# Performance work log

Hardware: AMD Instinct MI355X
Metric: run time of the kernel (lower is better)

Reference implementation:

```python
import jax, jax.numpy as jnp
import numpy as np

B, N, D = 8, 2048, 8        # batch, nodes, input_dim == hidden_dim
E, DEC = 8, 128             # embedding_dim, decoder_dim


def _leaky(x, slope):
    return jnp.where(x >= 0, x, slope * x)


def _sage(x, attn, inv_deg, w, b):
    # adj transposed on dims (1,2) then left-matmul: new[b,i,d] = sum_j attn[b,j,i] x[b,j,d]
    new_x = jnp.einsum('bji,bjd->bid', attn, x)
    new_x = jnp.matmul(inv_deg, new_x)
    new_x = jnp.matmul(new_x, w)
    self_x = jnp.matmul(x, b)
    c = jnp.concatenate([new_x, self_x], axis=2)
    norm = jnp.sqrt(jnp.sum(c * c, axis=2, keepdims=True))
    return c / jnp.maximum(norm, 1e-12)  # F.normalize(p=2, dim=2)


def setup_inputs():
    key = jax.random.key(0)
    ks = jax.random.split(key, 12)
    x = jax.random.normal(ks[0], (B, N, D), jnp.float32)
    adj = jax.random.randint(ks[1], (B, N, N), 0, 2).astype(jnp.int32)
    deg = jnp.sum(adj.astype(jnp.float32), axis=2)
    inv_deg = jax.vmap(jnp.diag)(1.0 / (deg + 1.0))  # [B,N,N] diagonal
    g = np.sqrt(2.0)  # xavier-style scale stand-in
    W = jax.random.normal(ks[2], (D, D), jnp.float32) * (g / np.sqrt(2 * D))
    a = jax.random.normal(ks[3], (2 * D, 1), jnp.float32) * (g / np.sqrt(2 * D + 1))
    w1 = jax.random.normal(ks[4], (D, D), jnp.float32) * 0.3
    b1 = jax.random.normal(ks[5], (D, D), jnp.float32) * 0.3
    w2 = jax.random.normal(ks[6], (2 * D, D), jnp.float32) * 0.3
    b2 = jax.random.normal(ks[7], (2 * D, D), jnp.float32) * 0.3
    w3 = jax.random.normal(ks[8], (2 * D, E), jnp.float32) * 0.3
    b3 = jax.random.normal(ks[9], (2 * D, E), jnp.float32) * 0.3
    P1 = jax.random.normal(ks[10], (2 * E, DEC), jnp.float32) * 0.1
    P2 = jax.random.normal(ks[11], (DEC, DEC), jnp.float32) * 0.1
    return {"x": x, "adj": adj, "inv_deg": inv_deg, "W": W, "a": a,
            "w1": w1, "b1": b1, "w2": w2, "b2": b2, "w3": w3, "b3": b3,
            "P1": P1, "P2": P2}


def reference(x, adj, inv_deg, W, a, w1, b1, w2, b2, w3, b3, P1, P2):
    h = jnp.matmul(x, W)                          # [B,N,D]
    # e[b,i,j] = leaky(h[b,i].a1 + h[b,j].a2), equivalent to cat+matmul without O(N^2*2D) tensor
    f1 = jnp.matmul(h, a[:D, 0])                  # [B,N]
    f2 = jnp.matmul(h, a[D:, 0])                  # [B,N]
    e = _leaky(f1[:, :, None] + f2[:, None, :], 0.2)
    e = jnp.where(adj > 0, e, jnp.float32(-9e15))
    attn = jax.nn.softmax(e, axis=2)              # [B,N,N]
    out = _leaky(_sage(x, attn, inv_deg, w1, b1), 0.1)
    out = _leaky(_sage(out, attn, inv_deg, w2, b2), 0.1)
    out = _leaky(_sage(out, attn, inv_deg, w3, b3), 0.1)
    da = out[:, N - 2]                            # [B,2E]
    db = out[:, N - 1]
    ypred = jnp.einsum('bi,id,de,je,bj->b', da, P1, P2, P1, db)
    return ypred[:, None]
```

## Files before the change

### kernel.cpp

```cpp
#include <hip/hip_runtime.h>
#include <math.h>

constexpr int CB   = 8;
constexpr int CN   = 2048;
constexpr int CD   = 8;
constexpr int CDEC = 128;
constexpr int CBN  = CB * CN;
constexpr int NWRD = CN / 64;
constexpr int JSP  = 32;
constexpr int JLEN = CN / JSP;

__device__ __forceinline__ float msel_s(unsigned long long m, float p) {
  float r;
  asm("v_cndmask_b32 %0, 0, %1, %2" : "=v"(r) : "v"(p), "s"(m));
  return r;
}
__device__ __forceinline__ float msel(unsigned long long m, int lane, float p) {
  return ((m >> lane) & 1ull) ? p : 0.f;
}

__global__ void prep_k(const float* __restrict__ x,
                       const float* __restrict__ W, const float* __restrict__ a,
                       const float* __restrict__ w1, const float* __restrict__ b1,
                       float4* __restrict__ pk, float4* __restrict__ qk,
                       float* __restrict__ feat1w, float* __restrict__ selfb1) {
  int t = blockIdx.x * blockDim.x + threadIdx.x;
  if (t >= CBN) return;
  const float* xr = x + (size_t)t * CD;
  float h[CD];
#pragma unroll
  for (int d = 0; d < CD; ++d) {
    float s = 0.f;
#pragma unroll
    for (int k = 0; k < CD; ++k) s = fmaf(xr[k], W[k * CD + d], s);
    h[d] = s;
  }
  float s1 = 0.f, s2 = 0.f;
#pragma unroll
  for (int d = 0; d < CD; ++d) { s1 = fmaf(h[d], a[d], s1); s2 = fmaf(h[d], a[CD + d], s2); }
  pk[t] = make_float4(s1, expf(s1), expf(0.2f * s1), 0.f);
  qk[t] = make_float4(s2, expf(s2), expf(0.2f * s2), 0.f);
  float fw[8], fb[8];
#pragma unroll
  for (int o = 0; o < 8; ++o) {
    float sw = 0.f, sb = 0.f;
#pragma unroll
    for (int d = 0; d < CD; ++d) {
      sw = fmaf(xr[d], w1[d * 8 + o], sw);
      sb = fmaf(xr[d], b1[d * 8 + o], sb);
    }
    fw[o] = sw; fb[o] = sb;
  }
  float4* f4 = (float4*)(feat1w + (size_t)t * 8);
  f4[0] = make_float4(fw[0], fw[1], fw[2], fw[3]);
  f4[1] = make_float4(fw[4], fw[5], fw[6], fw[7]);
  float4* s4 = (float4*)(selfb1 + (size_t)t * 8);
  s4[0] = make_float4(fb[0], fb[1], fb[2], fb[3]);
  s4[1] = make_float4(fb[4], fb[5], fb[6], fb[7]);
}

__global__ __launch_bounds__(256) void mask_k(const int* __restrict__ adj,
    float4* __restrict__ pk, const float4* __restrict__ qk,
    unsigned long long* __restrict__ maskT) {
  const int lane = threadIdx.x & 63;
  const int gw2 = blockIdx.x * 4 + (threadIdx.x >> 6);
  const int b = gw2 >> 9;
  const int jw = gw2 & 511;
  const int* ab = adj + (size_t)b * CN * CN;
  const float4* qb = qk + (size_t)b * CN;
  float f1[4];
#pragma unroll
  for (int r = 0; r < 4; ++r) f1[r] = pk[b * CN + jw + 512 * r].x;
  float A[4] = {0.f, 0.f, 0.f, 0.f}, C[4] = {0.f, 0.f, 0.f, 0.f};
  int deg[4] = {0, 0, 0, 0};
  for (int k = 0; k < NWRD; ++k) {
    int i = k * 64 + lane;
    float4 q = qb[i];
    unsigned long long m[4];
#pragma unroll
    for (int r = 0; r < 4; ++r) {
      bool bit = ab[(size_t)(jw + 512 * r) * CN + i] > 0;
      m[r] = __ballot(bit);
      bool cond = (f1[r] + q.x) >= 0.f;
      A[r] += (bit && cond) ? q.y : 0.f;
      C[r] += (bit && !cond) ? q.z : 0.f;
    }
    if (lane == 0) {
#pragma unroll
      for (int r = 0; r < 4; ++r) {
        maskT[((size_t)(b * NWRD + k)) * CN + jw + 512 * r] = m[r];
        deg[r] += __popcll(m[r]);
      }
    }
  }
#pragma unroll
  for (int r = 0; r < 4; ++r) {
#pragma unroll
    for (int off = 32; off; off >>= 1) {
      A[r] += __shfl_down(A[r], off);
      C[r] += __shfl_down(C[r], off);
    }
  }
  if (lane == 0) {
#pragma unroll
    for (int r = 0; r < 4; ++r) {
      int gr = b * CN + jw + 512 * r;
      float4 pj = pk[gr];
      float s = pj.y * A[r] + pj.z * C[r];
      float ga = (s > 0.f) ? pj.y / s : 0.f;
      float gb = (s > 0.f) ? pj.z / s : 0.f;
      float dv = 1.f / (float)(deg[r] + 1);
      pk[gr] = make_float4(pj.x, ga, gb, dv);
    }
  }
}

__global__ __launch_bounds__(256) void aggf_k(const float* __restrict__ feat,
                      const unsigned long long* __restrict__ maskT,
                      const float4* __restrict__ pk, const float4* __restrict__ qk,
                      float* __restrict__ part) {
  const int js = blockIdx.x, ic = blockIdx.y, b = blockIdx.z;
  const int t = threadIdx.x;
  const int w = __builtin_amdgcn_readfirstlane(t >> 6);
  const int i1 = ic * 512 + t, i2 = i1 + 256;
  const int gi1 = b * CN + i1, gi2 = b * CN + i2;
  float4 q1 = qk[gi1], q2 = qk[gi2];
  const unsigned long long* mc1 = maskT + ((size_t)(b * NWRD + ic * 8 + w)) * CN + js * JLEN;
  const unsigned long long* mc2 = maskT + ((size_t)(b * NWRD + ic * 8 + 4 + w)) * CN + js * JLEN;
  const float4* pb = pk + (size_t)b * CN + js * JLEN;
  const float* fb  = feat + ((size_t)b * CN + js * JLEN) * 8;
  float acc1[8], acc2[8];
#pragma unroll
  for (int d = 0; d < 8; ++d) { acc1[d] = 0.f; acc2[d] = 0.f; }
#pragma unroll 4
  for (int jj = 0; jj < JLEN; ++jj) {
    unsigned long long m1 = mc1[jj];
    unsigned long long m2 = mc2[jj];
    float4 pj = pb[jj];
    const float* fr = fb + jj * 8;
    float wA = msel_s(m1, fmaxf(pj.y * q1.y, pj.z * q1.z));
    float wB = msel_s(m2, fmaxf(pj.y * q2.y, pj.z * q2.z));
#pragma unroll
    for (int d = 0; d < 8; ++d) {
      acc1[d] = fmaf(wA, fr[d], acc1[d]);
      acc2[d] = fmaf(wB, fr[d], acc2[d]);
    }
  }
  float4* p1 = (float4*)(part + ((size_t)js * CBN + gi1) * 8);
  float4* p2 = (float4*)(part + ((size_t)js * CBN + gi2) * 8);
  p1[0] = make_float4(acc1[0], acc1[1], acc1[2], acc1[3]);
  p1[1] = make_float4(acc1[4], acc1[5], acc1[6], acc1[7]);
  p2[0] = make_float4(acc2[0], acc2[1], acc2[2], acc2[3]);
  p2[1] = make_float4(acc2[4], acc2[5], acc2[6], acc2[7]);
}

__global__ void epi8_k(const float* __restrict__ part, const float* __restrict__ selfb1,
                       const float4* __restrict__ pk,
                       const float* __restrict__ w2, const float* __restrict__ b2,
                       float* __restrict__ feat2w, float* __restrict__ selfb2) {
  int t = blockIdx.x * blockDim.x + threadIdx.x;
  if (t >= CBN) return;
  float4 a0 = make_float4(0.f, 0.f, 0.f, 0.f), a1 = a0;
  for (int p_ = 0; p_ < JSP; ++p_) {
    const float4* pr = (const float4*)(part + ((size_t)p_ * CBN + t) * 8);
    float4 r0 = pr[0], r1 = pr[1];
    a0.x += r0.x; a0.y += r0.y; a0.z += r0.z; a0.w += r0.w;
    a1.x += r1.x; a1.y += r1.y; a1.z += r1.z; a1.w += r1.w;
  }
  float di = pk[t].w;
  const float4* sb = (const float4*)(selfb1 + (size_t)t * 8);
  float4 s0 = sb[0], s1 = sb[1];
  float c[16] = {a0.x * di, a0.y * di, a0.z * di, a0.w * di,
                 a1.x * di, a1.y * di, a1.z * di, a1.w * di,
                 s0.x, s0.y, s0.z, s0.w, s1.x, s1.y, s1.z, s1.w};
  float nn = 0.f;
#pragma unroll
  for (int k = 0; k < 16; ++k) nn += c[k] * c[k];
  float inv = 1.f / fmaxf(sqrtf(nn), 1e-12f);
  float ff[16];
#pragma unroll
  for (int k = 0; k < 16; ++k) {
    float v = c[k] * inv;
    ff[k] = (v >= 0.f) ? v : 0.1f * v;
  }
  float fw[8], fb[8];
#pragma unroll
  for (int o = 0; o < 8; ++o) {
    float sw = 0.f, sb2_ = 0.f;
#pragma unroll
    for (int d = 0; d < 16; ++d) {
      sw = fmaf(ff[d], w2[d * 8 + o], sw);
      sb2_ = fmaf(ff[d], b2[d * 8 + o], sb2_);
    }
    fw[o] = sw; fb[o] = sb2_;
  }
  float4* f4 = (float4*)(feat2w + (size_t)t * 8);
  f4[0] = make_float4(fw[0], fw[1], fw[2], fw[3]);
  f4[1] = make_float4(fw[4], fw[5], fw[6], fw[7]);
  float4* s4 = (float4*)(selfb2 + (size_t)t * 8);
  s4[0] = make_float4(fb[0], fb[1], fb[2], fb[3]);
  s4[1] = make_float4(fb[4], fb[5], fb[6], fb[7]);
}

__global__ __launch_bounds__(256) void epi16f_k(
    const float* __restrict__ part2, const float* __restrict__ selfb2,
    const unsigned long long* __restrict__ maskT,
    const float4* __restrict__ pk, const float4* __restrict__ qk,
    float* __restrict__ gpart, float* __restrict__ self2) {
  __shared__ float redA[4][16], redB[4][16];
  const int t = threadIdx.x;
  const int lane = t & 63, wv = t >> 6;
  const int gr = blockIdx.x * 256 + t;
  const int b = blockIdx.x >> 3, blk8 = blockIdx.x & 7;
  const int j = gr - b * CN;
  const int ia = CN - 2, ib = CN - 1;
  float4 a0 = make_float4(0.f, 0.f, 0.f, 0.f), a1 = a0;
  for (int p = 0; p < JSP; ++p) {
    const float4* pr = (const float4*)(part2 + ((size_t)p * CBN + gr) * 8);
    float4 r0 = pr[0], r1 = pr[1];
    a0.x += r0.x; a0.y += r0.y; a0.z += r0.z; a0.w += r0.w;
    a1.x += r1.x; a1.y += r1.y; a1.z += r1.z; a1.w += r1.w;
  }
  float4 pj = pk[gr];
  const float4* sb = (const float4*)(selfb2 + (size_t)gr * 8);
  float4 s0 = sb[0], s1 = sb[1];
  float c[16] = {a0.x * pj.w, a0.y * pj.w, a0.z * pj.w, a0.w * pj.w,
                 a1.x * pj.w, a1.y * pj.w, a1.z * pj.w, a1.w * pj.w,
                 s0.x, s0.y, s0.z, s0.w, s1.x, s1.y, s1.z, s1.w};
  float nn = 0.f;
#pragma unroll
  for (int k = 0; k < 16; ++k) nn += c[k] * c[k];
  float inv = 1.f / fmaxf(sqrtf(nn), 1e-12f);
  float ff[16];
#pragma unroll
  for (int k = 0; k < 16; ++k) {
    float v = c[k] * inv;
    ff[k] = (v >= 0.f) ? v : 0.1f * v;
  }
  if (j == ia || j == ib) {
    float* s = self2 + ((size_t)b * 2 + (j == ib ? 1 : 0)) * 16;
#pragma unroll
    for (int d = 0; d < 16; ++d) s[d] = ff[d];
  }
  unsigned long long m = maskT[((size_t)(b * NWRD + (NWRD - 1))) * CN + j];
  float4 qa = qk[b * CN + ia], qb = qk[b * CN + ib];
  float wA = ((m >> 62) & 1ull) ? fmaxf(pj.y * qa.y, pj.z * qa.z) : 0.f;
  float wB = (m >> 63) ? fmaxf(pj.y * qb.y, pj.z * qb.z) : 0.f;
  float accA[16], accB[16];
#pragma unroll
  for (int d = 0; d < 16; ++d) { accA[d] = wA * ff[d]; accB[d] = wB * ff[d]; }
#pragma unroll
  for (int d = 0; d < 16; ++d) {
#pragma unroll
    for (int off = 32; off; off >>= 1) {
      accA[d] += __shfl_down(accA[d], off);
      accB[d] += __shfl_down(accB[d], off);
    }
  }
  if (lane == 0) {
#pragma unroll
    for (int d = 0; d < 16; ++d) { redA[wv][d] = accA[d]; redB[wv][d] = accB[d]; }
  }
  __syncthreads();
  if (t < 32) {
    int row = t >> 4, k = t & 15;
    float s = row ? (redB[0][k] + redB[1][k] + redB[2][k] + redB[3][k])
                  : (redA[0][k] + redA[1][k] + redA[2][k] + redA[3][k]);
    gpart[(((size_t)b * 8 + blk8) * 2 + row) * 16 + k] = s;
  }
}

__global__ __launch_bounds__(CDEC) void dec_k(
    const float* __restrict__ gpart, const float* __restrict__ self2,
    const float4* __restrict__ pk,
    const float* __restrict__ w3, const float* __restrict__ b3,
    const float* __restrict__ P1, const float* __restrict__ P2,
    float* __restrict__ y) {
  __shared__ float agA[16], agB[16], cA[16], cB[16], daF[16], dbF[16];
  __shared__ float vsh[CDEC], red[CDEC];
  const int b = blockIdx.x;
  const int t = threadIdx.x;
  const int ia = CN - 2, ib = CN - 1;
  if (t < 32) {
    int row = t >> 4, k = t & 15;
    float s = 0.f;
#pragma unroll
    for (int blk = 0; blk < 8; ++blk)
      s += gpart[(((size_t)b * 8 + blk) * 2 + row) * 16 + k];
    float dv = pk[b * CN + (row ? ib : ia)].w;
    (row ? agB : agA)[k] = s * dv;
  }
  __syncthreads();
  if (t < 32) {
    int row = t >> 4, k = t & 15;
    const float* ag = row ? agB : agA;
    const float* self = self2 + ((size_t)b * 2 + row) * 16;
    float s = 0.f;
    if (k < 8) {
#pragma unroll
      for (int d = 0; d < 16; ++d) s = fmaf(ag[d], w3[d * 8 + k], s);
    } else {
#pragma unroll
      for (int d = 0; d < 16; ++d) s = fmaf(self[d], b3[d * 8 + (k - 8)], s);
    }
    (row ? cB : cA)[k] = s;
  }
  __syncthreads();
  if (t < 32) {
    int row = t >> 4, k = t & 15;
    const float* c = row ? cB : cA;
    float nn = 0.f;
#pragma unroll
    for (int q = 0; q < 16; ++q) nn += c[q] * c[q];
    float inv = 1.f / fmaxf(sqrtf(nn), 1e-12f);
    float v = c[k] * inv;
    (row ? dbF : daF)[k] = (v >= 0.f) ? v : 0.1f * v;
  }
  __syncthreads();
  float ue = 0.f, ve = 0.f;
#pragma unroll
  for (int i = 0; i < 16; ++i) {
    ue = fmaf(daF[i], P1[i * CDEC + t], ue);
    ve = fmaf(dbF[i], P1[i * CDEC + t], ve);
  }
  vsh[t] = ve;
  __syncthreads();
  float s = 0.f;
  for (int e2 = 0; e2 < CDEC; ++e2) s = fmaf(P2[t * CDEC + e2], vsh[e2], s);
  red[t] = s * ue;
  __syncthreads();
  for (int off = 64; off; off >>= 1) {
    if (t < off) red[t] += red[t + off];
    __syncthreads();
  }
  if (t == 0) y[b] = red[0];
}

extern "C" void kernel_launch(void* const* d_in, const int* in_sizes, int n_in,
                              void* d_out, int out_size, void* d_ws, size_t ws_size,
                              hipStream_t stream) {
  const float* x  = (const float*)d_in[0];
  const int*   adj = (const int*)d_in[1];
  const float* W  = (const float*)d_in[3];
  const float* a  = (const float*)d_in[4];
  const float* w1 = (const float*)d_in[5];
  const float* b1 = (const float*)d_in[6];
  const float* w2 = (const float*)d_in[7];
  const float* b2 = (const float*)d_in[8];
  const float* w3 = (const float*)d_in[9];
  const float* b3 = (const float*)d_in[10];
  const float* P1 = (const float*)d_in[11];
  const float* P2 = (const float*)d_in[12];
  float* y = (float*)d_out;

  char* base = (char*)d_ws;
  size_t off = 0;
  auto alloc = [&](size_t bytes) -> void* {
    void* r = base + off;
    off += (bytes + 255) & ~(size_t)255;
    return r;
  };
  float4* pk = (float4*)alloc(sizeof(float4) * CBN);
  float4* qk = (float4*)alloc(sizeof(float4) * CBN);
  unsigned long long* maskT =
      (unsigned long long*)alloc(sizeof(unsigned long long) * (size_t)CBN * NWRD);
  float* feat1w = (float*)alloc(sizeof(float) * (size_t)CBN * 8);
  float* selfb1 = (float*)alloc(sizeof(float) * (size_t)CBN * 8);
  float* feat2w = (float*)alloc(sizeof(float) * (size_t)CBN * 8);
  float* selfb2 = (float*)alloc(sizeof(float) * (size_t)CBN * 8);
  float* part   = (float*)alloc(sizeof(float) * (size_t)JSP * CBN * 8);
  float* gpart  = (float*)alloc(sizeof(float) * CB * 8 * 2 * 16);
  float* self2  = (float*)alloc(sizeof(float) * CB * 2 * 16);

  hipLaunchKernelGGL(prep_k, dim3(CBN / 256), dim3(256), 0, stream,
                     x, W, a, w1, b1, pk, qk, feat1w, selfb1);
  hipLaunchKernelGGL(mask_k, dim3(1024), dim3(256), 0, stream, adj, pk, qk, maskT);
  hipLaunchKernelGGL(aggf_k, dim3(JSP, 4, CB), dim3(256), 0, stream, feat1w, maskT, pk, qk, part);
  hipLaunchKernelGGL(epi8_k, dim3(CBN / 256), dim3(256), 0, stream,
                     part, selfb1, pk, w2, b2, feat2w, selfb2);
  hipLaunchKernelGGL(aggf_k, dim3(JSP, 4, CB), dim3(256), 0, stream, feat2w, maskT, pk, qk, part);
  hipLaunchKernelGGL(epi16f_k, dim3(CBN / 256), dim3(256), 0, stream,
                     part, selfb2, maskT, pk, qk, gpart, self2);
  hipLaunchKernelGGL(dec_k, dim3(CB), dim3(CDEC), 0, stream,
                     gpart, self2, pk, w3, b3, P1, P2, y);
}
```

Baseline: 96.82 us.

## Fuse prep into mask kernel and decoder into last epilogue via counter

Merges the per-node projection kernel into the mask/softmax-stat kernel. Each block recomputes the q-side logits for the whole batch into shared memory instead of reading them from global memory. Also folds the decoder into the final epilogue: the last block per batch, found with an atomic counter and thread fences, runs the decoder. This removes two launches and the global round trip for q, at the cost of redundant per-block recomputation of 2048 node projections and a counter reset at the start of each run.

Result: slower. 111.2 us (+14.8%).

```diff
diff --git a/kernel.cpp b/kernel.cpp
--- a/kernel.cpp
+++ b/kernel.cpp
@@ -15,75 +15,91 @@
   asm("v_cndmask_b32 %0, 0, %1, %2" : "=v"(r) : "v"(p), "s"(m));
   return r;
 }
-__device__ __forceinline__ float msel(unsigned long long m, int lane, float p) {
-  return ((m >> lane) & 1ull) ? p : 0.f;
-}
-
-__global__ void prep_k(const float* __restrict__ x,
-                       const float* __restrict__ W, const float* __restrict__ a,
-                       const float* __restrict__ w1, const float* __restrict__ b1,
-                       float4* __restrict__ pk, float4* __restrict__ qk,
-                       float* __restrict__ feat1w, float* __restrict__ selfb1) {
-  int t = blockIdx.x * blockDim.x + threadIdx.x;
-  if (t >= CBN) return;
-  const float* xr = x + (size_t)t * CD;
-  float h[CD];
-#pragma unroll
-  for (int d = 0; d < CD; ++d) {
-    float s = 0.f;
-#pragma unroll
-    for (int k = 0; k < CD; ++k) s = fmaf(xr[k], W[k * CD + d], s);
-    h[d] = s;
-  }
-  float s1 = 0.f, s2 = 0.f;
-#pragma unroll
-  for (int d = 0; d < CD; ++d) { s1 = fmaf(h[d], a[d], s1); s2 = fmaf(h[d], a[CD + d], s2); }
-  pk[t] = make_float4(s1, expf(s1), expf(0.2f * s1), 0.f);
-  qk[t] = make_float4(s2, expf(s2), expf(0.2f * s2), 0.f);
-  float fw[8], fb[8];
-#pragma unroll
-  for (int o = 0; o < 8; ++o) {
+
+__global__ __launch_bounds__(256) void pmask_k(
+    const float* __restrict__ x, const int* __restrict__ adj,
+    const float* __restrict__ W, const float* __restrict__ a,
+    const float* __restrict__ w1, const float* __restrict__ b1,
+    float4* __restrict__ pk, float4* __restrict__ qk,
+    float* __restrict__ feat1w, float* __restrict__ selfb1,
+    unsigned long long* __restrict__ maskT, int* __restrict__ cnt) {
+  __shared__ float qf[CN], qE[CN], qF[CN];
+  __shared__ float p1f[16], p1E[16], p1F[16];
+  const int t = threadIdx.x;
+  const int lane = t & 63, wv = t >> 6;
+  const int bid = blockIdx.x;
+  const int b = bid >> 7;
+  const int bb = bid & 127;
+  const float* xb = x + (size_t)b * CN * CD;
+  if (bid == 0 && t < CB) cnt[t] = 0;
+  for (int s = 0; s < 8; ++s) {
+    int n = t + 256 * s;
+    const float* xr = xb + (size_t)n * CD;
+    float h[CD];
+#pragma unroll
+    for (int d = 0; d < CD; ++d) {
+      float acc = 0.f;
+#pragma unroll
+      for (int k = 0; k < CD; ++k) acc = fmaf(xr[k], W[k * CD + d], acc);
+      h[d] = acc;
+    }
+    float s2 = 0.f;
+#pragma unroll
+    for (int d = 0; d < CD; ++d) s2 = fmaf(h[d], a[CD + d], s2);
+    qf[n] = s2; qE[n] = expf(s2); qF[n] = expf(0.2f * s2);
+  }
+  if (t < 16) {
+    int j = bb * 4 + (t & 3) + 512 * (t >> 2);
+    const float* xr = xb + (size_t)j * CD;
+    float h[CD];
+#pragma unroll
+    for (int d = 0; d < CD; ++d) {
+      float acc = 0.f;
+#pragma unroll
+      for (int k = 0; k < CD; ++k) acc = fmaf(xr[k], W[k * CD + d], acc);
+      h[d] = acc;
+    }
+    float s1 = 0.f;
+#pragma unroll
+    for (int d = 0; d < CD; ++d) s1 = fmaf(h[d], a[d], s1);
+    p1f[t] = s1; p1E[t] = expf(s1); p1F[t] = expf(0.2f * s1);
+  }
+  __syncthreads();
+  if (t < 16) {
+    int n = bb * 16 + t;
+    qk[b * CN + n] = make_float4(qf[n], qE[n], qF[n], 0.f);
+  }
+  if (t < 128) {
+    int n = bb * 16 + (t >> 3);
+    int o = t & 7;
+    const float* xr = xb + (size_t)n * CD;
     float sw = 0.f, sb = 0.f;
 #pragma unroll
     for (int d = 0; d < CD; ++d) {
       sw = fmaf(xr[d], w1[d * 8 + o], sw);
       sb = fmaf(xr[d], b1[d * 8 + o], sb);
     }
-    fw[o] = sw; fb[o] = sb;
-  }
-  float4* f4 = (float4*)(feat1w + (size_t)t * 8);
-  f4[0] = make_float4(fw[0], fw[1], fw[2], fw[3]);
-  f4[1] = make_float4(fw[4], fw[5], fw[6], fw[7]);
-  float4* s4 = (float4*)(selfb1 + (size_t)t * 8);
-  s4[0] = make_float4(fb[0], fb[1], fb[2], fb[3]);
-  s4[1] = make_float4(fb[4], fb[5], fb[6], fb[7]);
-}
-
-__global__ __launch_bounds__(256) void mask_k(const int* __restrict__ adj,
-    float4* __restrict__ pk, const float4* __restrict__ qk,
-    unsigned long long* __restrict__ maskT) {
-  const int lane = threadIdx.x & 63;
-  const int gw2 = blockIdx.x * 4 + (threadIdx.x >> 6);
-  const int b = gw2 >> 9;
-  const int jw = gw2 & 511;
+    feat1w[((size_t)(b * CN + n)) * 8 + o] = sw;
+    selfb1[((size_t)(b * CN + n)) * 8 + o] = sb;
+  }
+  const int jw = bb * 4 + wv;
   const int* ab = adj + (size_t)b * CN * CN;
-  const float4* qb = qk + (size_t)b * CN;
   float f1[4];
 #pragma unroll
-  for (int r = 0; r < 4; ++r) f1[r] = pk[b * CN + jw + 512 * r].x;
+  for (int r = 0; r < 4; ++r) f1[r] = p1f[r * 4 + wv];
   float A[4] = {0.f, 0.f, 0.f, 0.f}, C[4] = {0.f, 0.f, 0.f, 0.f};
   int deg[4] = {0, 0, 0, 0};
   for (int k = 0; k < NWRD; ++k) {
     int i = k * 64 + lane;
-    float4 q = qb[i];
+    float qx = qf[i], qy = qE[i], qz = qF[i];
     unsigned long long m[4];
 #pragma unroll
     for (int r = 0; r < 4; ++r) {
       bool bit = ab[(size_t)(jw + 512 * r) * CN + i] > 0;
       m[r] = __ballot(bit);
-      bool cond = (f1[r] + q.x) >= 0.f;
-      A[r] += (bit && cond) ? q.y : 0.f;
-      C[r] += (bit && !cond) ? q.z : 0.f;
+      bool cond = (f1[r] + qx) >= 0.f;
+      A[r] += (bit && cond) ? qy : 0.f;
+      C[r] += (bit && !cond) ? qz : 0.f;
     }
     if (lane == 0) {
 #pragma unroll
@@ -105,12 +121,12 @@
 #pragma unroll
     for (int r = 0; r < 4; ++r) {
       int gr = b * CN + jw + 512 * r;
-      float4 pj = pk[gr];
-      float s = pj.y * A[r] + pj.z * C[r];
-      float ga = (s > 0.f) ? pj.y / s : 0.f;
-      float gb = (s > 0.f) ? pj.z / s : 0.f;
+      float E1 = p1E[r * 4 + wv], F1 = p1F[r * 4 + wv];
+      float s = E1 * A[r] + F1 * C[r];
+      float ga = (s > 0.f) ? E1 / s : 0.f;
+      float gb = (s > 0.f) ? F1 / s : 0.f;
       float dv = 1.f / (float)(deg[r] + 1);
-      pk[gr] = make_float4(pj.x, ga, gb, dv);
+      pk[gr] = make_float4(p1f[r * 4 + wv], ga, gb, dv);
     }
   }
 }
@@ -202,11 +218,14 @@
   s4[1] = make_float4(fb[4], fb[5], fb[6], fb[7]);
 }
 
-__global__ __launch_bounds__(256) void epi16f_k(
+__global__ __launch_bounds__(256) void epi16fd_k(
     const float* __restrict__ part2, const float* __restrict__ selfb2,
     const unsigned long long* __restrict__ maskT,
     const float4* __restrict__ pk, const float4* __restrict__ qk,
-    float* __restrict__ gpart, float* __restrict__ self2) {
+    float* __restrict__ gpart, float* __restrict__ self2, int* __restrict__ cnt,
+    const float* __restrict__ w3, const float* __restrict__ b3,
+    const float* __restrict__ P1, const float* __restrict__ P2,
+    float* __restrict__ y) {
   __shared__ float redA[4][16], redB[4][16];
   const int t = threadIdx.x;
   const int lane = t & 63, wv = t >> 6;
@@ -268,19 +287,15 @@
                   : (redA[0][k] + redA[1][k] + redA[2][k] + redA[3][k]);
     gpart[(((size_t)b * 8 + blk8) * 2 + row) * 16 + k] = s;
   }
-}
-
-__global__ __launch_bounds__(CDEC) void dec_k(
-    const float* __restrict__ gpart, const float* __restrict__ self2,
-    const float4* __restrict__ pk,
-    const float* __restrict__ w3, const float* __restrict__ b3,
-    const float* __restrict__ P1, const float* __restrict__ P2,
-    float* __restrict__ y) {
+  __threadfence();
+  __syncthreads();
+  __shared__ int isLast;
+  if (t == 0) isLast = (atomicAdd(&cnt[b], 1) == 7) ? 1 : 0;
+  __syncthreads();
+  if (!isLast) return;
+  __threadfence();
   __shared__ float agA[16], agB[16], cA[16], cB[16], daF[16], dbF[16];
   __shared__ float vsh[CDEC], red[CDEC];
-  const int b = blockIdx.x;
-  const int t = threadIdx.x;
-  const int ia = CN - 2, ib = CN - 1;
   if (t < 32) {
     int row = t >> 4, k = t & 15;
     float s = 0.f;
@@ -308,26 +323,30 @@
   __syncthreads();
   if (t < 32) {
     int row = t >> 4, k = t & 15;
-    const float* c = row ? cB : cA;
-    float nn = 0.f;
-#pragma unroll
-    for (int q = 0; q < 16; ++q) nn += c[q] * c[q];
-    float inv = 1.f / fmaxf(sqrtf(nn), 1e-12f);
-    float v = c[k] * inv;
+    const float* cc = row ? cB : cA;
+    float nn2 = 0.f;
+#pragma unroll
+    for (int q = 0; q < 16; ++q) nn2 += cc[q] * cc[q];
+    float inv2 = 1.f / fmaxf(sqrtf(nn2), 1e-12f);
+    float v = cc[k] * inv2;
     (row ? dbF : daF)[k] = (v >= 0.f) ? v : 0.1f * v;
   }
   __syncthreads();
   float ue = 0.f, ve = 0.f;
-#pragma unroll
-  for (int i = 0; i < 16; ++i) {
-    ue = fmaf(daF[i], P1[i * CDEC + t], ue);
-    ve = fmaf(dbF[i], P1[i * CDEC + t], ve);
-  }
-  vsh[t] = ve;
-  __syncthreads();
-  float s = 0.f;
-  for (int e2 = 0; e2 < CDEC; ++e2) s = fmaf(P2[t * CDEC + e2], vsh[e2], s);
-  red[t] = s * ue;
+  if (t < CDEC) {
+#pragma unroll
+    for (int i = 0; i < 16; ++i) {
+      ue = fmaf(daF[i], P1[i * CDEC + t], ue);
+      ve = fmaf(dbF[i], P1[i * CDEC + t], ve);
+    }
+    vsh[t] = ve;
+  }
+  __syncthreads();
+  if (t < CDEC) {
+    float s = 0.f;
+    for (int e2 = 0; e2 < CDEC; ++e2) s = fmaf(P2[t * CDEC + e2], vsh[e2], s);
+    red[t] = s * ue;
+  }
   __syncthreads();
   for (int off = 64; off; off >>= 1) {
     if (t < off) red[t] += red[t + off];
@@ -371,16 +390,14 @@
   float* part   = (float*)alloc(sizeof(float) * (size_t)JSP * CBN * 8);
   float* gpart  = (float*)alloc(sizeof(float) * CB * 8 * 2 * 16);
   float* self2  = (float*)alloc(sizeof(float) * CB * 2 * 16);
-
-  hipLaunchKernelGGL(prep_k, dim3(CBN / 256), dim3(256), 0, stream,
-                     x, W, a, w1, b1, pk, qk, feat1w, selfb1);
-  hipLaunchKernelGGL(mask_k, dim3(1024), dim3(256), 0, stream, adj, pk, qk, maskT);
+  int*   cnt    = (int*)alloc(sizeof(int) * CB);
+
+  hipLaunchKernelGGL(pmask_k, dim3(1024), dim3(256), 0, stream,
+                     x, adj, W, a, w1, b1, pk, qk, feat1w, selfb1, maskT, cnt);
   hipLaunchKernelGGL(aggf_k, dim3(JSP, 4, CB), dim3(256), 0, stream, feat1w, maskT, pk, qk, part);
   hipLaunchKernelGGL(epi8_k, dim3(CBN / 256), dim3(256), 0, stream,
                      part, selfb1, pk, w2, b2, feat2w, selfb2);
   hipLaunchKernelGGL(aggf_k, dim3(JSP, 4, CB), dim3(256), 0, stream, feat2w, maskT, pk, qk, part);
-  hipLaunchKernelGGL(epi16f_k, dim3(CBN / 256), dim3(256), 0, stream,
-                     part, selfb2, maskT, pk, qk, gpart, self2);
-  hipLaunchKernelGGL(dec_k, dim3(CB), dim3(CDEC), 0, stream,
-                     gpart, self2, pk, w3, b3, P1, P2, y);
-}
+  hipLaunchKernelGGL(epi16fd_k, dim3(CBN / 256), dim3(256), 0, stream,
+                     part, selfb2, maskT, pk, qk, gpart, self2, cnt, w3, b3, P1, P2, y);
+}
```
